# Kernel optimization log

Measured on AMD Instinct MI355X. Metric: run time of the kernel, lower is better.

Reference implementation:

```python
import jax, jax.numpy as jnp
import numpy as np

B, T, D, K = 16, 2048, 256, 1024


def setup_inputs() -> dict:
    key = jax.random.key(0)
    k1, k2 = jax.random.split(key)
    z_e_x = jax.random.normal(k1, (B, T, D), dtype=jnp.float32)
    # torch init is uniform(-1/K, 1/K); use normal scaled similarly for a realistic trained codebook
    embedding = jax.random.normal(k2, (K, D), dtype=jnp.float32)
    return {"z_e_x": z_e_x, "embedding": embedding}


def _vq_indices(inputs_flat, codebook):
    codebook_sqr = jnp.sum(codebook * codebook, axis=1)            # [K]
    inputs_sqr = jnp.sum(inputs_flat * inputs_flat, axis=1, keepdims=True)  # [N,1]
    distances = inputs_sqr + codebook_sqr[None, :] - 2.0 * (inputs_flat @ codebook.T)  # [N,K]
    return jnp.argmin(distances, axis=1)                           # [N] int


def reference(z_e_x, embedding):
    Dd = embedding.shape[1]
    inputs_flat = z_e_x.reshape(-1, Dd)                 # [N, D]
    indices_flat = _vq_indices(inputs_flat, embedding)  # [N]
    codes = embedding[indices_flat].reshape(z_e_x.shape)  # gather lookup
    z_q_x = codes                                       # straight-through quantized output
    z_q_x_bar = codes                                   # eval mode: embedding unchanged, same gather
    indices = indices_flat.reshape(z_e_x.shape[:-1])
    return (z_q_x, z_q_x_bar, indices)
```

## Files before the change

### kernel.cpp

```cpp
#include <hip/hip_runtime.h>
#include <float.h>

constexpr int kD = 256;
constexpr int kK = 1024;
constexpr int kN = 16 * 2048;

using bf16x8 = __attribute__((ext_vector_type(8))) short;
using f32x16 = __attribute__((ext_vector_type(16))) float;
using u16x8  = __attribute__((ext_vector_type(8))) unsigned short;

__device__ __forceinline__ unsigned short f2bf(float x) {
    union { float f; unsigned u; } a; a.f = x;
    const unsigned u = a.u;
    return (unsigned short)((u + 0x7fffu + ((u >> 16) & 1u)) >> 16);
}
__device__ __forceinline__ float bf2f(unsigned short b) {
    union { unsigned u; float f; } a; a.u = ((unsigned)b) << 16;
    return a.f;
}

#define GLOAD_LDS16(GP, LP) \
    __builtin_amdgcn_global_load_lds((const __attribute__((address_space(1))) unsigned int*)(GP), \
                                     (__attribute__((address_space(3))) unsigned int*)(LP), 16, 0, 0)

__global__ void vq_split_kernel(const float* __restrict__ src,
                                unsigned short* __restrict__ oh,
                                unsigned short* __restrict__ om,
                                unsigned short* __restrict__ ol) {
    const int RB = blockIdx.x;
    const int t  = threadIdx.x;
    #pragma unroll
    for (int it = 0; it < 8; ++it) {
        const int u   = it * 256 + t;
        const int l   = u & 63;
        const int f   = (u >> 6) & 1;
        const int t16 = u >> 7;
        const int row = RB * 64 + f * 32 + (l & 31);
        const int d0  = t16 * 16 + (l >> 5) * 8;
        const float4 v0 = *reinterpret_cast<const float4*>(src + (size_t)row * kD + d0);
        const float4 v1 = *reinterpret_cast<const float4*>(src + (size_t)row * kD + d0 + 4);
        const float x[8] = {v0.x, v0.y, v0.z, v0.w, v1.x, v1.y, v1.z, v1.w};
        u16x8 H, M, L;
        #pragma unroll
        for (int e = 0; e < 8; ++e) {
            const unsigned short h = f2bf(x[e]);
            const float r1 = x[e] - bf2f(h);
            const unsigned short m = f2bf(r1);
            const float r2 = r1 - bf2f(m);
            const unsigned short lo = f2bf(r2);
            H[e] = (short)h; M[e] = (short)m; L[e] = (short)lo;
        }
        const size_t o = (size_t)RB * 16384 + (size_t)u * 8;
        *reinterpret_cast<u16x8*>(oh + o) = H;
        *reinterpret_cast<u16x8*>(om + o) = M;
        *reinterpret_cast<u16x8*>(ol + o) = L;
    }
}

__global__ void vq_split_csqr_kernel(const float* __restrict__ src,
                                     unsigned short* __restrict__ oh,
                                     unsigned short* __restrict__ om,
                                     unsigned short* __restrict__ ol,
                                     float* __restrict__ csqr) {
    __shared__ float part[64][4];
    const int RB = blockIdx.x;
    const int t  = threadIdx.x;
    #pragma unroll
    for (int it = 0; it < 8; ++it) {
        const int u   = it * 256 + t;
        const int l   = u & 63;
        const int f   = (u >> 6) & 1;
        const int t16 = u >> 7;
        const int row = RB * 64 + f * 32 + (l & 31);
        const int d0  = t16 * 16 + (l >> 5) * 8;
        const float4 v0 = *reinterpret_cast<const float4*>(src + (size_t)row * kD + d0);
        const float4 v1 = *reinterpret_cast<const float4*>(src + (size_t)row * kD + d0 + 4);
        const float x[8] = {v0.x, v0.y, v0.z, v0.w, v1.x, v1.y, v1.z, v1.w};
        u16x8 H, M, L;
        #pragma unroll
        for (int e = 0; e < 8; ++e) {
            const unsigned short h = f2bf(x[e]);
            const float r1 = x[e] - bf2f(h);
            const unsigned short m = f2bf(r1);
            const float r2 = r1 - bf2f(m);
            const unsigned short lo = f2bf(r2);
            H[e] = (short)h; M[e] = (short)m; L[e] = (short)lo;
        }
        const size_t o = (size_t)RB * 16384 + (size_t)u * 8;
        *reinterpret_cast<u16x8*>(oh + o) = H;
        *reinterpret_cast<u16x8*>(om + o) = M;
        *reinterpret_cast<u16x8*>(ol + o) = L;
    }
    const int r = t >> 2, q = t & 3;
    const float* rp = src + (size_t)(RB * 64 + r) * kD + q * 64;
    float s = 0.0f;
    #pragma unroll
    for (int i = 0; i < 16; ++i) {
        const float4 v = reinterpret_cast<const float4*>(rp)[i];
        s += v.x * v.x + v.y * v.y + v.z * v.z + v.w * v.w;
    }
    part[r][q] = s;
    __syncthreads();
    if (t < 64) csqr[RB * 64 + t] = part[t][0] + part[t][1] + part[t][2] + part[t][3];
}

__global__ __launch_bounds__(256, 2) void vq_gemm_kernel(
    const unsigned short* __restrict__ xh, const unsigned short* __restrict__ xm,
    const unsigned short* __restrict__ xl,
    const unsigned short* __restrict__ eh, const unsigned short* __restrict__ em,
    const unsigned short* __restrict__ el,
    const float* __restrict__ csqr,
    float* __restrict__ cand_val, int* __restrict__ cand_idx)
{
    __shared__ bf16x8 smem[2][2304];
    const int tid  = threadIdx.x;
    const int lane = tid & 63;
    const int wid  = tid >> 6;
    const int wr   = wid >> 1;
    const int wc   = wid & 1;

    const int w    = blockIdx.x;
    const int xcd  = w & 7;
    const int slot = w >> 3;
    const int rbp  = xcd * 16 + (slot >> 3);
    const int cbp  = slot & 7;

    const unsigned short* gbase[9];
    int ldsoff[9];
    #pragma unroll
    for (int k2 = 0; k2 < 9; ++k2) {
        const int s = wid * 9 + k2;
        const bool isB = s >= 24;
        const int q   = isB ? s - 24 : s;
        const int grp = q / 6;
        const int rem = q % 6;
        const int f   = rem / 3;
        const int lv  = rem % 3;
        const unsigned short* img = isB ? (lv == 0 ? eh : lv == 1 ? em : el)
                                        : (lv == 0 ? xh : lv == 1 ? xm : xl);
        const int RBx = isB ? (cbp * 2 + grp) : (rbp * 4 + grp);
        gbase[k2] = img + (size_t)RBx * 16384 + f * 512 + lane * 8;
        ldsoff[k2] = (isB ? 1536 + q * 64 : q * 64);
    }

    f32x16 acc[4][2];
    #pragma unroll
    for (int m = 0; m < 4; ++m) { acc[m][0] = (f32x16)0.0f; acc[m][1] = (f32x16)0.0f; }

    int au[4], bu[2];
    #pragma unroll
    for (int m = 0; m < 4; ++m) au[m] = ((wr * 2 + (m >> 1)) * 6 + (m & 1) * 3) * 64 + lane;
    #pragma unroll
    for (int n = 0; n < 2; ++n) bu[n] = 1536 + (wc * 6 + n * 3) * 64 + lane;

    #pragma unroll
    for (int k2 = 0; k2 < 9; ++k2) GLOAD_LDS16(gbase[k2], &smem[0][ldsoff[k2]]);
    __syncthreads();

    for (int c = 0; c < 16; ++c) {
        const int cur = c & 1;
        if (c < 15) {
            #pragma unroll
            for (int k2 = 0; k2 < 9; ++k2)
                GLOAD_LDS16(gbase[k2] + (size_t)(c + 1) * 1024, &smem[cur ^ 1][ldsoff[k2]]);
        }
        const bf16x8* sb = smem[cur];
        bf16x8 A[3][4];
        #pragma unroll
        for (int m = 0; m < 4; ++m) {
            A[0][m] = sb[au[m]]; A[1][m] = sb[au[m] + 64]; A[2][m] = sb[au[m] + 128];
        }
#define MFMA(a, b, cacc) __builtin_amdgcn_mfma_f32_32x32x16_bf16(a, b, cacc, 0, 0, 0)
        #pragma unroll
        for (int n = 0; n < 2; ++n) {
            const bf16x8 bh = sb[bu[n]], bm = sb[bu[n] + 64], bl = sb[bu[n] + 128];
            #pragma unroll
            for (int m = 0; m < 4; ++m) {
                f32x16 a5 = acc[m][n];
                a5 = MFMA(A[0][m], bh, a5);
                a5 = MFMA(A[0][m], bm, a5);
                a5 = MFMA(A[1][m], bh, a5);
                a5 = MFMA(A[0][m], bl, a5);
                a5 = MFMA(A[2][m], bh, a5);
                a5 = MFMA(A[1][m], bm, a5);
                acc[m][n] = a5;
            }
        }
#undef MFMA
        __syncthreads();
    }

    const int colbase = cbp * 128 + wc * 64;
    const float cs0 = csqr[colbase + (lane & 31)];
    const float cs1 = csqr[colbase + 32 + (lane & 31)];
    const int rowbase = rbp * 256 + wr * 128 + 4 * (lane >> 5);
    const int cslot = cbp * 2 + wc;

    #pragma unroll
    for (int m = 0; m < 4; ++m) {
        #pragma unroll
        for (int r = 0; r < 16; ++r) {
            float bv = fmaf(-2.0f, acc[m][0][r], cs0);
            int   bi = colbase + (lane & 31);
            const float v1 = fmaf(-2.0f, acc[m][1][r], cs1);
            if (v1 < bv) { bv = v1; bi = colbase + 32 + (lane & 31); }
            #pragma unroll
            for (int mk = 16; mk >= 1; mk >>= 1) {
                const float ov = __shfl_xor(bv, mk);
                const int   oi = __shfl_xor(bi, mk);
                if (ov < bv || (ov == bv && oi < bi)) { bv = ov; bi = oi; }
            }
            if ((lane & 31) == 0) {
                const int row = rowbase + m * 32 + (r & 3) + 8 * (r >> 2);
                cand_val[(size_t)cslot * kN + row] = bv;
                cand_idx[(size_t)cslot * kN + row] = bi;
            }
        }
    }
}

__global__ void vq_combine_kernel(const float* __restrict__ cand_val,
                                  const int* __restrict__ cand_idx,
                                  int* __restrict__ idx, float* __restrict__ idxf)
{
    const int row = blockIdx.x * 256 + threadIdx.x;
    float bv = cand_val[row];
    int   bi = cand_idx[row];
    #pragma unroll
    for (int s = 1; s < 16; ++s) {
        const float v = cand_val[(size_t)s * kN + row];
        const int  i2 = cand_idx[(size_t)s * kN + row];
        if (v < bv || (v == bv && i2 < bi)) { bv = v; bi = i2; }
    }
    idx[row]  = bi;
    idxf[row] = (float)bi;
}

__global__ void vq_gather_kernel(const float* __restrict__ E, const int* __restrict__ idx,
                                 float* __restrict__ zq, float* __restrict__ zqb) {
    const int row = blockIdx.x * 4 + (threadIdx.x >> 6);
    const int lane = threadIdx.x & 63;
    const int k = idx[row];
    const float4 v = reinterpret_cast<const float4*>(E + (size_t)k * kD)[lane];
    reinterpret_cast<float4*>(zq + (size_t)row * kD)[lane] = v;
    reinterpret_cast<float4*>(zqb + (size_t)row * kD)[lane] = v;
}

extern "C" void kernel_launch(void* const* d_in, const int* in_sizes, int n_in,
                              void* d_out, int out_size, void* d_ws, size_t ws_size,
                              hipStream_t stream) {
    const float* X = (const float*)d_in[0];
    const float* E = (const float*)d_in[1];

    float* out  = (float*)d_out;
    float* zq   = out;
    float* zqb  = out + (size_t)kN * kD;
    float* idxf = out + 2 * (size_t)kN * kD;

    char* ob = (char*)d_out;
    unsigned short* XIh = (unsigned short*)ob;
    unsigned short* XIm = XIh + (size_t)kN * kD;
    unsigned short* XIl = XIm + (size_t)kN * kD;
    float* cand_val = (float*)(ob + 3ull * kN * kD * 2);
    int*   cand_idx = (int*)(ob + 3ull * kN * kD * 2 + 16ull * kN * 4);

    char* ws = (char*)d_ws;
    float* csqr = (float*)ws;
    unsigned short* EIh = (unsigned short*)(ws + 4096);
    unsigned short* EIm = EIh + (size_t)kK * kD;
    unsigned short* EIl = EIm + (size_t)kK * kD;
    int* idx = (int*)(ws + 4096 + 3ull * kK * kD * 2);

    vq_split_kernel<<<kN / 64, 256, 0, stream>>>(X, XIh, XIm, XIl);
    vq_split_csqr_kernel<<<kK / 64, 256, 0, stream>>>(E, EIh, EIm, EIl, csqr);
    vq_gemm_kernel<<<(kN / 256) * (kK / 128), 256, 0, stream>>>(
        XIh, XIm, XIl, EIh, EIm, EIl, csqr, cand_val, cand_idx);
    vq_combine_kernel<<<kN / 256, 256, 0, stream>>>(cand_val, cand_idx, idx, idxf);
    vq_gather_kernel<<<kN / 4, 256, 0, stream>>>(E, idx, zq, zqb);
}
```

Before: 255.5 us.

## Fuse split kernels, use atomicMin row keys, and pipeline GEMM loads

Merges the X and codebook split kernels into one launch. It replaces the candidate-buffer-plus-combine pass with a 64-bit atomicMin on an order-preserving (distance, index) key per row, and the gather kernel now writes the float indices too. The GEMM main loop now keeps two chunks of loads in flight using explicit vmcnt waits and barriers, and raises wave priority during the MFMA section. In exchange it adds a memset and atomic traffic, and ties rely on the packed key keeping the smallest index.

```diff
diff --git a/kernel.cpp b/kernel.cpp
--- a/kernel.cpp
+++ b/kernel.cpp
@@ -23,12 +23,21 @@
     __builtin_amdgcn_global_load_lds((const __attribute__((address_space(1))) unsigned int*)(GP), \
                                      (__attribute__((address_space(3))) unsigned int*)(LP), 16, 0, 0)
 
-__global__ void vq_split_kernel(const float* __restrict__ src,
-                                unsigned short* __restrict__ oh,
-                                unsigned short* __restrict__ om,
-                                unsigned short* __restrict__ ol) {
-    const int RB = blockIdx.x;
-    const int t  = threadIdx.x;
+__global__ void vq_split_all_kernel(const float* __restrict__ X, const float* __restrict__ E,
+                                    unsigned short* __restrict__ xh, unsigned short* __restrict__ xm,
+                                    unsigned short* __restrict__ xl,
+                                    unsigned short* __restrict__ eh, unsigned short* __restrict__ em,
+                                    unsigned short* __restrict__ el,
+                                    float* __restrict__ csqr) {
+    __shared__ float part[64][4];
+    const int b   = blockIdx.x;
+    const bool isE = b >= 512;
+    const int RB  = isE ? b - 512 : b;
+    const float* src = isE ? E : X;
+    unsigned short* oh = isE ? eh : xh;
+    unsigned short* om = isE ? em : xm;
+    unsigned short* ol = isE ? el : xl;
+    const int t = threadIdx.x;
     #pragma unroll
     for (int it = 0; it < 8; ++it) {
         const int u   = it * 256 + t;
@@ -55,53 +64,19 @@
         *reinterpret_cast<u16x8*>(om + o) = M;
         *reinterpret_cast<u16x8*>(ol + o) = L;
     }
-}
-
-__global__ void vq_split_csqr_kernel(const float* __restrict__ src,
-                                     unsigned short* __restrict__ oh,
-                                     unsigned short* __restrict__ om,
-                                     unsigned short* __restrict__ ol,
-                                     float* __restrict__ csqr) {
-    __shared__ float part[64][4];
-    const int RB = blockIdx.x;
-    const int t  = threadIdx.x;
-    #pragma unroll
-    for (int it = 0; it < 8; ++it) {
-        const int u   = it * 256 + t;
-        const int l   = u & 63;
-        const int f   = (u >> 6) & 1;
-        const int t16 = u >> 7;
-        const int row = RB * 64 + f * 32 + (l & 31);
-        const int d0  = t16 * 16 + (l >> 5) * 8;
-        const float4 v0 = *reinterpret_cast<const float4*>(src + (size_t)row * kD + d0);
-        const float4 v1 = *reinterpret_cast<const float4*>(src + (size_t)row * kD + d0 + 4);
-        const float x[8] = {v0.x, v0.y, v0.z, v0.w, v1.x, v1.y, v1.z, v1.w};
-        u16x8 H, M, L;
-        #pragma unroll
-        for (int e = 0; e < 8; ++e) {
-            const unsigned short h = f2bf(x[e]);
-            const float r1 = x[e] - bf2f(h);
-            const unsigned short m = f2bf(r1);
-            const float r2 = r1 - bf2f(m);
-            const unsigned short lo = f2bf(r2);
-            H[e] = (short)h; M[e] = (short)m; L[e] = (short)lo;
-        }
-        const size_t o = (size_t)RB * 16384 + (size_t)u * 8;
-        *reinterpret_cast<u16x8*>(oh + o) = H;
-        *reinterpret_cast<u16x8*>(om + o) = M;
-        *reinterpret_cast<u16x8*>(ol + o) = L;
-    }
-    const int r = t >> 2, q = t & 3;
-    const float* rp = src + (size_t)(RB * 64 + r) * kD + q * 64;
-    float s = 0.0f;
-    #pragma unroll
-    for (int i = 0; i < 16; ++i) {
-        const float4 v = reinterpret_cast<const float4*>(rp)[i];
-        s += v.x * v.x + v.y * v.y + v.z * v.z + v.w * v.w;
-    }
-    part[r][q] = s;
-    __syncthreads();
-    if (t < 64) csqr[RB * 64 + t] = part[t][0] + part[t][1] + part[t][2] + part[t][3];
+    if (isE) {
+        const int r = t >> 2, q = t & 3;
+        const float* rp = E + (size_t)(RB * 64 + r) * kD + q * 64;
+        float s = 0.0f;
+        #pragma unroll
+        for (int i = 0; i < 16; ++i) {
+            const float4 v = reinterpret_cast<const float4*>(rp)[i];
+            s += v.x * v.x + v.y * v.y + v.z * v.z + v.w * v.w;
+        }
+        part[r][q] = s;
+        __syncthreads();
+        if (t < 64) csqr[RB * 64 + t] = part[t][0] + part[t][1] + part[t][2] + part[t][3];
+    }
 }
 
 __global__ __launch_bounds__(256, 2) void vq_gemm_kernel(
@@ -110,7 +85,7 @@
     const unsigned short* __restrict__ eh, const unsigned short* __restrict__ em,
     const unsigned short* __restrict__ el,
     const float* __restrict__ csqr,
-    float* __restrict__ cand_val, int* __restrict__ cand_idx)
+    unsigned long long* __restrict__ rowkey)
 {
     __shared__ bf16x8 smem[2][2304];
     const int tid  = threadIdx.x;
@@ -153,97 +128,102 @@
     #pragma unroll
     for (int n = 0; n < 2; ++n) bu[n] = 1536 + (wc * 6 + n * 3) * 64 + lane;
 
-    #pragma unroll
-    for (int k2 = 0; k2 < 9; ++k2) GLOAD_LDS16(gbase[k2], &smem[0][ldsoff[k2]]);
-    __syncthreads();
-
-    for (int c = 0; c < 16; ++c) {
-        const int cur = c & 1;
-        if (c < 15) {
-            #pragma unroll
-            for (int k2 = 0; k2 < 9; ++k2)
-                GLOAD_LDS16(gbase[k2] + (size_t)(c + 1) * 1024, &smem[cur ^ 1][ldsoff[k2]]);
-        }
-        const bf16x8* sb = smem[cur];
-        bf16x8 A[3][4];
+#define MFMA(a, b, cacc) __builtin_amdgcn_mfma_f32_32x32x16_bf16(a, b, cacc, 0, 0, 0)
+    auto compute_chunk = [&](const bf16x8* sb) {
+        bf16x8 A0[4], A1[4], A2[4];
         #pragma unroll
         for (int m = 0; m < 4; ++m) {
-            A[0][m] = sb[au[m]]; A[1][m] = sb[au[m] + 64]; A[2][m] = sb[au[m] + 128];
-        }
-#define MFMA(a, b, cacc) __builtin_amdgcn_mfma_f32_32x32x16_bf16(a, b, cacc, 0, 0, 0)
+            A0[m] = sb[au[m]]; A1[m] = sb[au[m] + 64]; A2[m] = sb[au[m] + 128];
+        }
+        __builtin_amdgcn_s_setprio(1);
         #pragma unroll
         for (int n = 0; n < 2; ++n) {
             const bf16x8 bh = sb[bu[n]], bm = sb[bu[n] + 64], bl = sb[bu[n] + 128];
             #pragma unroll
             for (int m = 0; m < 4; ++m) {
                 f32x16 a5 = acc[m][n];
-                a5 = MFMA(A[0][m], bh, a5);
-                a5 = MFMA(A[0][m], bm, a5);
-                a5 = MFMA(A[1][m], bh, a5);
-                a5 = MFMA(A[0][m], bl, a5);
-                a5 = MFMA(A[2][m], bh, a5);
-                a5 = MFMA(A[1][m], bm, a5);
+                a5 = MFMA(A0[m], bh, a5);
+                a5 = MFMA(A0[m], bm, a5);
+                a5 = MFMA(A1[m], bh, a5);
+                a5 = MFMA(A0[m], bl, a5);
+                a5 = MFMA(A2[m], bh, a5);
+                a5 = MFMA(A1[m], bm, a5);
                 acc[m][n] = a5;
             }
         }
+        __builtin_amdgcn_s_setprio(0);
+    };
 #undef MFMA
-        __syncthreads();
-    }
-
+#define MFMA(a, b, cacc) __builtin_amdgcn_mfma_f32_32x32x16_bf16(a, b, cacc, 0, 0, 0)
+
+    #pragma unroll
+    for (int k2 = 0; k2 < 9; ++k2) GLOAD_LDS16(gbase[k2], &smem[0][ldsoff[k2]]);
+    #pragma unroll
+    for (int k2 = 0; k2 < 9; ++k2) GLOAD_LDS16(gbase[k2] + 1024, &smem[1][ldsoff[k2]]);
+
+    #pragma unroll 1
+    for (int c = 0; c < 15; ++c) {
+        const int cur = c & 1;
+        asm volatile("s_waitcnt vmcnt(9)" ::: "memory");
+        __builtin_amdgcn_s_barrier();
+        asm volatile("" ::: "memory");
+        compute_chunk(smem[cur]);
+        asm volatile("" ::: "memory");
+        __builtin_amdgcn_s_barrier();
+        asm volatile("" ::: "memory");
+        if (c < 14) {
+            #pragma unroll
+            for (int k2 = 0; k2 < 9; ++k2)
+                GLOAD_LDS16(gbase[k2] + (size_t)(c + 2) * 1024, &smem[cur][ldsoff[k2]]);
+        }
+    }
+    asm volatile("s_waitcnt vmcnt(0)" ::: "memory");
+    __builtin_amdgcn_s_barrier();
+    asm volatile("" ::: "memory");
+    compute_chunk(smem[1]);
+#undef MFMA
+
+    const int lane31 = lane & 31;
     const int colbase = cbp * 128 + wc * 64;
-    const float cs0 = csqr[colbase + (lane & 31)];
-    const float cs1 = csqr[colbase + 32 + (lane & 31)];
+    const float cs0 = csqr[colbase + lane31];
+    const float cs1 = csqr[colbase + 32 + lane31];
     const int rowbase = rbp * 256 + wr * 128 + 4 * (lane >> 5);
-    const int cslot = cbp * 2 + wc;
 
     #pragma unroll
     for (int m = 0; m < 4; ++m) {
         #pragma unroll
         for (int r = 0; r < 16; ++r) {
             float bv = fmaf(-2.0f, acc[m][0][r], cs0);
-            int   bi = colbase + (lane & 31);
+            int   bi = colbase + lane31;
             const float v1 = fmaf(-2.0f, acc[m][1][r], cs1);
-            if (v1 < bv) { bv = v1; bi = colbase + 32 + (lane & 31); }
+            if (v1 < bv) { bv = v1; bi = colbase + 32 + lane31; }
             #pragma unroll
             for (int mk = 16; mk >= 1; mk >>= 1) {
                 const float ov = __shfl_xor(bv, mk);
                 const int   oi = __shfl_xor(bi, mk);
                 if (ov < bv || (ov == bv && oi < bi)) { bv = ov; bi = oi; }
             }
-            if ((lane & 31) == 0) {
+            if (lane31 == 0) {
                 const int row = rowbase + m * 32 + (r & 3) + 8 * (r >> 2);
-                cand_val[(size_t)cslot * kN + row] = bv;
-                cand_idx[(size_t)cslot * kN + row] = bi;
+                unsigned kb = __float_as_uint(bv);
+                kb = (bv < 0.0f) ? ~kb : (kb | 0x80000000u);
+                atomicMin(&rowkey[row], ((unsigned long long)kb << 32) | (unsigned)bi);
             }
         }
     }
 }
 
-__global__ void vq_combine_kernel(const float* __restrict__ cand_val,
-                                  const int* __restrict__ cand_idx,
-                                  int* __restrict__ idx, float* __restrict__ idxf)
-{
-    const int row = blockIdx.x * 256 + threadIdx.x;
-    float bv = cand_val[row];
-    int   bi = cand_idx[row];
-    #pragma unroll
-    for (int s = 1; s < 16; ++s) {
-        const float v = cand_val[(size_t)s * kN + row];
-        const int  i2 = cand_idx[(size_t)s * kN + row];
-        if (v < bv || (v == bv && i2 < bi)) { bv = v; bi = i2; }
-    }
-    idx[row]  = bi;
-    idxf[row] = (float)bi;
-}
-
-__global__ void vq_gather_kernel(const float* __restrict__ E, const int* __restrict__ idx,
-                                 float* __restrict__ zq, float* __restrict__ zqb) {
+__global__ void vq_gather_kernel(const float* __restrict__ E,
+                                 const unsigned long long* __restrict__ rowkey,
+                                 float* __restrict__ zq, float* __restrict__ zqb,
+                                 float* __restrict__ idxf) {
     const int row = blockIdx.x * 4 + (threadIdx.x >> 6);
     const int lane = threadIdx.x & 63;
-    const int k = idx[row];
+    const unsigned k = (unsigned)(rowkey[row] & 0xFFFFFFFFull);
     const float4 v = reinterpret_cast<const float4*>(E + (size_t)k * kD)[lane];
     reinterpret_cast<float4*>(zq + (size_t)row * kD)[lane] = v;
     reinterpret_cast<float4*>(zqb + (size_t)row * kD)[lane] = v;
+    if (lane == 0) idxf[row] = (float)k;
 }
 
 extern "C" void kernel_launch(void* const* d_in, const int* in_sizes, int n_in,
@@ -261,20 +241,18 @@
     unsigned short* XIh = (unsigned short*)ob;
     unsigned short* XIm = XIh + (size_t)kN * kD;
     unsigned short* XIl = XIm + (size_t)kN * kD;
-    float* cand_val = (float*)(ob + 3ull * kN * kD * 2);
-    int*   cand_idx = (int*)(ob + 3ull * kN * kD * 2 + 16ull * kN * 4);
 
     char* ws = (char*)d_ws;
-    float* csqr = (float*)ws;
-    unsigned short* EIh = (unsigned short*)(ws + 4096);
+    unsigned long long* rowkey = (unsigned long long*)ws;
+    float* csqr = (float*)(ws + (size_t)kN * 8);
+    unsigned short* EIh = (unsigned short*)(ws + (size_t)kN * 8 + 4096);
     unsigned short* EIm = EIh + (size_t)kK * kD;
     unsigned short* EIl = EIm + (size_t)kK * kD;
-    int* idx = (int*)(ws + 4096 + 3ull * kK * kD * 2);
-
-    vq_split_kernel<<<kN / 64, 256, 0, stream>>>(X, XIh, XIm, XIl);
-    vq_split_csqr_kernel<<<kK / 64, 256, 0, stream>>>(E, EIh, EIm, EIl, csqr);
+
+    hipMemsetAsync(rowkey, 0xFF, (size_t)kN * 8, stream);
+    vq_split_all_kernel<<<kN / 64 + kK / 64, 256, 0, stream>>>(
+        X, E, XIh, XIm, XIl, EIh, EIm, EIl, csqr);
     vq_gemm_kernel<<<(kN / 256) * (kK / 128), 256, 0, stream>>>(
-        XIh, XIm, XIl, EIh, EIm, EIl, csqr, cand_val, cand_idx);
-    vq_combine_kernel<<<kN / 256, 256, 0, stream>>>(cand_val, cand_idx, idx, idxf);
-    vq_gather_kernel<<<kN / 4, 256, 0, stream>>>(E, idx, zq, zqb);
-}
+        XIh, XIm, XIl, EIh, EIm, EIl, csqr, rowkey);
+    vq_gather_kernel<<<kN / 4, 256, 0, stream>>>(E, rowkey, zq, zqb, idxf);
+}
```

After: 250.7 us. No clear change (-1.9%).
